# Kernel tuning notes

Hardware: AMD Instinct MI355X
Metric: run time of the kernel (lower is better)

Reference implementation:

```python
import jax, jax.numpy as jnp
import numpy as np

N = 50000
E = 800000
IN = 128
HID = 32
HEADS = 4
OUT = 32
NEG_SLOPE = 0.2  # PyG GATConv default


def setup_inputs() -> dict:
    key = jax.random.key(0)
    ks = jax.random.split(key, 16)
    s = lambda k, sh: jax.random.normal(k, sh, jnp.float32) * 0.05
    inp = {}
    inp["x"] = jax.random.normal(ks[0], (N, IN), jnp.float32)
    inp["edge_idx"] = jax.random.randint(ks[1], (2, E), 0, N)
    inp["edge_attr"] = jax.random.normal(ks[2], (E, 1), jnp.float32)
    inp["lin1_w"] = s(ks[3], (IN, HEADS * HID))
    inp["att1_src"] = s(ks[4], (HEADS, HID))
    inp["att1_dst"] = s(ks[5], (HEADS, HID))
    inp["lin1_edge_w"] = s(ks[6], (1, HEADS * HID))
    inp["att1_edge"] = s(ks[7], (HEADS, HID))
    inp["bias1"] = jnp.zeros((HEADS * HID,), jnp.float32)
    inp["lin2_w"] = s(ks[8], (HEADS * HID, OUT))
    inp["att2_src"] = s(ks[9], (1, OUT))
    inp["att2_dst"] = s(ks[10], (1, OUT))
    inp["lin2_edge_w"] = s(ks[11], (1, OUT))
    inp["att2_edge"] = s(ks[12], (1, OUT))
    inp["bias2"] = jnp.zeros((OUT,), jnp.float32)
    return inp


def _gat_conv(x, src, dst, eattr, lin_w, a_src, a_dst, lin_e, a_e, bias, heads, ch, concat):
    """PyG GATConv (eval mode): gather -> leaky_relu logits -> segment softmax over dst -> scatter-sum."""
    n = x.shape[0]
    xl = (x @ lin_w).reshape(n, heads, ch)                      # [N,H,C]
    alpha = ((xl * a_src).sum(-1)[src]                          # [Etot,H]
             + (xl * a_dst).sum(-1)[dst]
             + ((eattr @ lin_e).reshape(-1, heads, ch) * a_e).sum(-1))
    alpha = jax.nn.leaky_relu(alpha, NEG_SLOPE)
    amax = jax.ops.segment_max(alpha, dst, num_segments=n)      # every node has a self-loop
    ex = jnp.exp(alpha - amax[dst])
    den = jax.ops.segment_sum(ex, dst, num_segments=n)
    w = ex / den[dst]                                           # [Etot,H]
    out = jax.ops.segment_sum(w[:, :, None] * xl[src], dst, num_segments=n)  # [N,H,C]
    out = out.reshape(n, heads * ch) if concat else out.mean(axis=1)
    return out + bias


def reference(x, edge_idx, edge_attr,
              lin1_w, att1_src, att1_dst, lin1_edge_w, att1_edge, bias1,
              lin2_w, att2_src, att2_dst, lin2_edge_w, att2_edge, bias2):
    n = x.shape[0]
    # add_self_loops=True with edge_attr fill_value='mean' (PyG default when edge_dim is set)
    loops = jnp.arange(n)
    src = jnp.concatenate([edge_idx[0], loops])
    dst = jnp.concatenate([edge_idx[1], loops])
    ea = jnp.concatenate(
        [edge_attr, jnp.broadcast_to(edge_attr.mean(0, keepdims=True), (n, edge_attr.shape[1]))], 0)
    h = jax.nn.elu(_gat_conv(x, src, dst, ea, lin1_w, att1_src, att1_dst,
                             lin1_edge_w, att1_edge, bias1, HEADS, HID, True))
    # F.dropout with training=False -> identity (eval mode)
    return _gat_conv(h, src, dst, ea, lin2_w, att2_src, att2_dst,
                     lin2_edge_w, att2_edge, bias2, 1, OUT, True)
```

## Files before the change

### kernel.cpp

```cpp
#include <hip/hip_runtime.h>
#include <hip/hip_fp16.h>
#include <math.h>

#define NN   50000
#define EE   800000
#define ETOT 850000
#define NEG  0.2f
#define SCAN_BLOCKS ((NN + 255) / 256)

#define O_DEG    0
#define O_EASUM  50000
#define ZERO_ELEMS 50004
#define O_COEF   50004
#define O_ROWPTR 50012
#define O_CURSOR 100016
#define O_BLKSUM 150016
#define O_BLKOFF 150272
#define O_CSRSE  150528
#define O_ASRC1  1850528
#define O_ADST1  2050528
#define O_XLH    2250528
#define O_OUT1   5450528
#define O_HLH    11850528
#define O_ASRC2  12650528
#define O_ADST2  12700528
#define WS_ELEMS 12750528

__global__ __launch_bounds__(256) void k_ea_count(
    const float* __restrict__ ea, const int* __restrict__ ei,
    float* __restrict__ easum, int* __restrict__ deg) {
  __shared__ float red[4];
  int e = blockIdx.x * 256 + threadIdx.x;
  float s = 0.f;
  if (e < EE) {
    s = ea[e];
    atomicAdd(deg + ei[EE + e], 1);
  }
  #pragma unroll
  for (int o = 32; o > 0; o >>= 1) s += __shfl_down(s, o, 64);
  if ((threadIdx.x & 63) == 0) red[threadIdx.x >> 6] = s;
  __syncthreads();
  if (threadIdx.x == 0) atomicAdd(easum, red[0] + red[1] + red[2] + red[3]);
}

__global__ void k_coef(const float* __restrict__ lew1, const float* __restrict__ ae1,
                       const float* __restrict__ lew2, const float* __restrict__ ae2,
                       float* __restrict__ coef) {
  int t = threadIdx.x;
  float p = lew1[t] * ae1[t];
  #pragma unroll
  for (int o = 16; o > 0; o >>= 1) p += __shfl_down(p, o, 32);
  if ((t & 31) == 0) coef[t >> 5] = p;
  if (t < 32) {
    float q = lew2[t] * ae2[t];
    #pragma unroll
    for (int o = 16; o > 0; o >>= 1) q += __shfl_down(q, o, 32);
    if (t == 0) coef[4] = q;
  }
}

__device__ __forceinline__ int wave_incl_scan(int v, int lane) {
  #pragma unroll
  for (int o = 1; o < 64; o <<= 1) {
    int u = __shfl_up(v, o, 64);
    if (lane >= o) v += u;
  }
  return v;
}

__global__ __launch_bounds__(256) void k_scan_blk(const int* __restrict__ deg,
                                                  int* __restrict__ rowptr,
                                                  int* __restrict__ blksum) {
  __shared__ int wsum[4];
  const int t = threadIdx.x;
  const int i = blockIdx.x * 256 + t;
  const int lane = t & 63, wv = t >> 6;
  int v = (i < NN) ? (deg[i] + 1) : 0;
  int incl = wave_incl_scan(v, lane);
  if (lane == 63) wsum[wv] = incl;
  __syncthreads();
  int off = 0;
  #pragma unroll
  for (int k = 0; k < 4; ++k) if (k < wv) off += wsum[k];
  incl += off;
  if (i < NN) rowptr[i] = incl - v;
  if (t == 255) blksum[blockIdx.x] = incl;
}

__global__ __launch_bounds__(256) void k_scan_top(const int* __restrict__ blksum,
                                                  int* __restrict__ blkoff) {
  __shared__ int wsum[4];
  const int t = threadIdx.x;
  const int lane = t & 63, wv = t >> 6;
  int v = (t < SCAN_BLOCKS) ? blksum[t] : 0;
  int incl = wave_incl_scan(v, lane);
  if (lane == 63) wsum[wv] = incl;
  __syncthreads();
  int off = 0;
  #pragma unroll
  for (int k = 0; k < 4; ++k) if (k < wv) off += wsum[k];
  incl += off;
  if (t < SCAN_BLOCKS) blkoff[t] = incl - v;
}

__global__ __launch_bounds__(256) void k_scan_add(int* __restrict__ rowptr,
                                                  int* __restrict__ cursor,
                                                  const int* __restrict__ blkoff) {
  const int i = blockIdx.x * 256 + threadIdx.x;
  if (i < NN) {
    int r = rowptr[i] + blkoff[blockIdx.x];
    rowptr[i] = r;
    cursor[i] = r;
  }
  if (i == 0) rowptr[NN] = ETOT;
}

__global__ void k_fill(const int* __restrict__ ei, const float* __restrict__ eattr,
                       const float* __restrict__ easum, int* __restrict__ cursor,
                       uint2* __restrict__ csr_se) {
  int e = blockIdx.x * 256 + threadIdx.x;
  if (e >= ETOT) return;
  int s, d; float ea;
  if (e < EE) { s = ei[e]; d = ei[EE + e]; ea = eattr[e]; }
  else { s = d = e - EE; ea = easum[0] * (1.f / EE); }
  int slot = atomicAdd(cursor + d, 1);
  csr_se[slot] = make_uint2((unsigned)s, __float_as_uint(ea));
}

#define GEMM_STEP(WB, K, XS) {                                              \
    const float4* Wr = (const float4*)((WB) + (size_t)(K));                 \
    _Pragma("unroll")                                                       \
    for (int j4 = 0; j4 < 8; ++j4) {                                        \
      float4 wv = Wr[j4];                                                   \
      acc[j4 * 4 + 0] += (XS) * wv.x;                                       \
      acc[j4 * 4 + 1] += (XS) * wv.y;                                       \
      acc[j4 * 4 + 2] += (XS) * wv.z;                                       \
      acc[j4 * 4 + 3] += (XS) * wv.w;                                       \
    } }

#define L1_NB ((NN + 63) / 64)
__global__ __launch_bounds__(64) void k_lin1(
    const float* __restrict__ x, const float* __restrict__ W,
    const float* __restrict__ att_src, const float* __restrict__ att_dst,
    __half* __restrict__ xlh, float* __restrict__ asrc, float* __restrict__ adst) {
  const int bid = blockIdx.x;
  const int h   = bid / L1_NB;
  const int n   = (bid % L1_NB) * 64 + threadIdx.x;
  const int nc  = n < NN ? n : NN - 1;
  const float4* xr = (const float4*)(x + (size_t)nc * 128);
  const float*  Wh = W + h * 32;
  float acc[32];
  #pragma unroll
  for (int j = 0; j < 32; ++j) acc[j] = 0.f;
  float4 xv = xr[0];
  for (int kt = 0; kt < 32; ++kt) {
    float4 cur = xv;
    if (kt < 31) xv = xr[kt + 1];
    GEMM_STEP(Wh, (kt * 4 + 0) * 128, cur.x);
    GEMM_STEP(Wh, (kt * 4 + 1) * 128, cur.y);
    GEMM_STEP(Wh, (kt * 4 + 2) * 128, cur.z);
    GEMM_STEP(Wh, (kt * 4 + 3) * 128, cur.w);
  }
  if (n < NN) {
    __align__(16) __half hbuf[32];
    #pragma unroll
    for (int j = 0; j < 32; ++j) hbuf[j] = __float2half_rn(acc[j]);
    float4* dst = (float4*)(xlh + (size_t)n * 128 + h * 32);
    #pragma unroll
    for (int i = 0; i < 4; ++i) dst[i] = ((const float4*)hbuf)[i];
    float ss = 0.f, sd = 0.f;
    #pragma unroll
    for (int j = 0; j < 32; ++j) {
      ss += acc[j] * att_src[h * 32 + j];
      sd += acc[j] * att_dst[h * 32 + j];
    }
    asrc[n * 4 + h] = ss;
    adst[n * 4 + h] = sd;
  }
}

__global__ __launch_bounds__(256) void k_agg1(
    const int* __restrict__ rowptr, const uint2* __restrict__ csr_se,
    const float* __restrict__ asrc, const float* __restrict__ adst,
    const float* __restrict__ coef,
    const __half* __restrict__ xlh, float* __restrict__ out1) {
  int n = blockIdx.x * 8 + (threadIdx.x >> 5);
  if (n >= NN) return;
  int l = threadIdx.x & 31;
  int c4 = l << 2;
  int h = l >> 3;
  float cf = coef[h];
  float ad = adst[(size_t)n * 4 + h];
  int r0 = rowptr[n], r1 = rowptr[n + 1];
  float a0 = 0.f, a1 = 0.f, a2 = 0.f, a3 = 0.f, den = 0.f;
  for (int j = r0; j < r1; j += 4) {
    int sv[4]; float eav[4], asv[4]; uint2 raw[4];
    #pragma unroll
    for (int k = 0; k < 4; ++k) {
      int jj = (j + k < r1) ? (j + k) : (r1 - 1);
      uint2 se = csr_se[jj];
      sv[k] = (int)se.x;
      eav[k] = __uint_as_float(se.y);
    }
    #pragma unroll
    for (int k = 0; k < 4; ++k) {
      asv[k] = asrc[(size_t)sv[k] * 4 + h];
      raw[k] = *(const uint2*)(xlh + (size_t)sv[k] * 128 + c4);
    }
    #pragma unroll
    for (int k = 0; k < 4; ++k) {
      float alpha = asv[k] + ad + eav[k] * cf;
      alpha = alpha > 0.f ? alpha : NEG * alpha;
      float ex = (j + k < r1) ? __expf(alpha) : 0.f;
      __half2 p0, p1;
      *(unsigned int*)&p0 = raw[k].x;
      *(unsigned int*)&p1 = raw[k].y;
      float2 f0 = __half22float2(p0), f1 = __half22float2(p1);
      a0 += ex * f0.x;
      a1 += ex * f0.y;
      a2 += ex * f1.x;
      a3 += ex * f1.y;
      den += ex;
    }
  }
  float inv = 1.f / den;
  *(float4*)(out1 + (size_t)n * 128 + c4) = make_float4(a0 * inv, a1 * inv, a2 * inv, a3 * inv);
}

__global__ __launch_bounds__(64) void k_lin2(
    const float* __restrict__ out1, const float* __restrict__ bias1,
    const float* __restrict__ W2,
    const float* __restrict__ as2w, const float* __restrict__ ad2w,
    __half* __restrict__ hlh, float* __restrict__ asrc2, float* __restrict__ adst2) {
  const int n  = blockIdx.x * 64 + threadIdx.x;
  const int nc = n < NN ? n : NN - 1;
  const float4* xr = (const float4*)(out1 + (size_t)nc * 128);
  const float4* br = (const float4*)bias1;
  float acc[32];
  #pragma unroll
  for (int j = 0; j < 32; ++j) acc[j] = 0.f;
  float4 xv = xr[0];
  for (int kt = 0; kt < 32; ++kt) {
    float4 cur = xv;
    if (kt < 31) xv = xr[kt + 1];
    float4 b = br[kt];
    cur.x += b.x; cur.y += b.y; cur.z += b.z; cur.w += b.w;
    cur.x = cur.x > 0.f ? cur.x : (expf(cur.x) - 1.f);
    cur.y = cur.y > 0.f ? cur.y : (expf(cur.y) - 1.f);
    cur.z = cur.z > 0.f ? cur.z : (expf(cur.z) - 1.f);
    cur.w = cur.w > 0.f ? cur.w : (expf(cur.w) - 1.f);
    GEMM_STEP(W2, (kt * 4 + 0) * 32, cur.x);
    GEMM_STEP(W2, (kt * 4 + 1) * 32, cur.y);
    GEMM_STEP(W2, (kt * 4 + 2) * 32, cur.z);
    GEMM_STEP(W2, (kt * 4 + 3) * 32, cur.w);
  }
  if (n < NN) {
    __align__(16) __half hbuf[32];
    #pragma unroll
    for (int j = 0; j < 32; ++j) hbuf[j] = __float2half_rn(acc[j]);
    float4* dst = (float4*)(hlh + (size_t)n * 32);
    #pragma unroll
    for (int i = 0; i < 4; ++i) dst[i] = ((const float4*)hbuf)[i];
    float ps = 0.f, pd = 0.f;
    #pragma unroll
    for (int j = 0; j < 32; ++j) {
      ps += acc[j] * as2w[j];
      pd += acc[j] * ad2w[j];
    }
    asrc2[n] = ps;
    adst2[n] = pd;
  }
}

__global__ __launch_bounds__(256) void k_agg2(
    const int* __restrict__ rowptr, const uint2* __restrict__ csr_se,
    const float* __restrict__ asrc2, const float* __restrict__ adst2,
    const float* __restrict__ coef,
    const __half* __restrict__ hlh, const float* __restrict__ bias2,
    float* __restrict__ out) {
  int n = blockIdx.x * 32 + (threadIdx.x >> 3);
  if (n >= NN) return;
  int c4 = (threadIdx.x & 7) << 2;
  float cf = coef[4];
  float ad = adst2[n];
  int r0 = rowptr[n], r1 = rowptr[n + 1];
  float a0 = 0.f, a1 = 0.f, a2 = 0.f, a3 = 0.f, den = 0.f;
  for (int j = r0; j < r1; j += 4) {
    int sv[4]; float eav[4], asv[4]; uint2 raw[4];
    #pragma unroll
    for (int k = 0; k < 4; ++k) {
      int jj = (j + k < r1) ? (j + k) : (r1 - 1);
      uint2 se = csr_se[jj];
      sv[k] = (int)se.x;
      eav[k] = __uint_as_float(se.y);
    }
    #pragma unroll
    for (int k = 0; k < 4; ++k) {
      asv[k] = asrc2[sv[k]];
      raw[k] = *(const uint2*)(hlh + (size_t)sv[k] * 32 + c4);
    }
    #pragma unroll
    for (int k = 0; k < 4; ++k) {
      float alpha = asv[k] + ad + eav[k] * cf;
      alpha = alpha > 0.f ? alpha : NEG * alpha;
      float ex = (j + k < r1) ? __expf(alpha) : 0.f;
      __half2 p0, p1;
      *(unsigned int*)&p0 = raw[k].x;
      *(unsigned int*)&p1 = raw[k].y;
      float2 f0 = __half22float2(p0), f1 = __half22float2(p1);
      a0 += ex * f0.x;
      a1 += ex * f0.y;
      a2 += ex * f1.x;
      a3 += ex * f1.y;
      den += ex;
    }
  }
  float inv = 1.f / den;
  float4 b = *(const float4*)(bias2 + c4);
  *(float4*)(out + (size_t)n * 32 + c4) =
      make_float4(a0 * inv + b.x, a1 * inv + b.y, a2 * inv + b.z, a3 * inv + b.w);
}

extern "C" void kernel_launch(void* const* d_in, const int* in_sizes, int n_in,
                              void* d_out, int out_size, void* d_ws, size_t ws_size,
                              hipStream_t stream) {
  const float* x        = (const float*)d_in[0];
  const int*   ei       = (const int*)d_in[1];
  const float* eattr    = (const float*)d_in[2];
  const float* lin1_w   = (const float*)d_in[3];
  const float* att1_src = (const float*)d_in[4];
  const float* att1_dst = (const float*)d_in[5];
  const float* lin1_ew  = (const float*)d_in[6];
  const float* att1_e   = (const float*)d_in[7];
  const float* bias1    = (const float*)d_in[8];
  const float* lin2_w   = (const float*)d_in[9];
  const float* att2_src = (const float*)d_in[10];
  const float* att2_dst = (const float*)d_in[11];
  const float* lin2_ew  = (const float*)d_in[12];
  const float* att2_e   = (const float*)d_in[13];
  const float* bias2    = (const float*)d_in[14];
  float* out = (float*)d_out;
  float* ws  = (float*)d_ws;
  int*   wsi = (int*)d_ws;

  int*    deg     = wsi + O_DEG;
  float*  easum   = ws + O_EASUM;
  float*  coef    = ws + O_COEF;
  int*    rowptr  = wsi + O_ROWPTR;
  int*    cursor  = wsi + O_CURSOR;
  int*    blksum  = wsi + O_BLKSUM;
  int*    blkoff  = wsi + O_BLKOFF;
  uint2*  csr_se  = (uint2*)(wsi + O_CSRSE);
  float*  asrc1   = ws + O_ASRC1;
  float*  adst1   = ws + O_ADST1;
  __half* xlh     = (__half*)(ws + O_XLH);
  float*  out1    = ws + O_OUT1;
  __half* hlh     = (__half*)(ws + O_HLH);
  float*  asrc2   = ws + O_ASRC2;
  float*  adst2   = ws + O_ADST2;

  hipMemsetAsync(ws, 0, (size_t)ZERO_ELEMS * sizeof(float), stream);

  k_ea_count<<<(EE + 255) / 256, 256, 0, stream>>>(eattr, ei, easum, deg);
  k_coef<<<1, 128, 0, stream>>>(lin1_ew, att1_e, lin2_ew, att2_e, coef);

  k_scan_blk<<<SCAN_BLOCKS, 256, 0, stream>>>(deg, rowptr, blksum);
  k_scan_top<<<1, 256, 0, stream>>>(blksum, blkoff);
  k_scan_add<<<SCAN_BLOCKS, 256, 0, stream>>>(rowptr, cursor, blkoff);
  k_fill<<<(ETOT + 255) / 256, 256, 0, stream>>>(ei, eattr, easum, cursor, csr_se);

  k_lin1<<<L1_NB * 4, 64, 0, stream>>>(x, lin1_w, att1_src, att1_dst, xlh, asrc1, adst1);
  k_agg1<<<(NN + 7) / 8, 256, 0, stream>>>(rowptr, csr_se, asrc1, adst1, coef, xlh, out1);

  k_lin2<<<(NN + 63) / 64, 64, 0, stream>>>(out1, bias1, lin2_w, att2_src, att2_dst, hlh, asrc2, adst2);
  k_agg2<<<(NN + 31) / 32, 256, 0, stream>>>(rowptr, csr_se, asrc2, adst2, coef, hlh, bias2, out);
}
```

Baseline: 346.6 us.

## Fuse all GAT stages into one cooperative persistent kernel with grid syncs

Replaces the chain of separate launches (memset, degree count, coef, three-stage scan, CSR fill, lin1, agg1, lin2, agg2) with a single cooperative kernel whose phases are separated by grid-wide syncs. The degree-count atomics now also record each edge's rank, so CSR slots are computed directly and the fill needs no second atomic pass. That fill is interleaved per wave with the lin1 GEMM tasks so the two overlap. The CSR is split into separate source and edge-attribute arrays. The aim is to remove per-launch overhead and the extra atomic traffic. The cost is about nine grid barriers, occupancy capped by launch bounds, and two gathers per edge instead of one packed load.

```diff
diff --git a/kernel.cpp b/kernel.cpp
--- a/kernel.cpp
+++ b/kernel.cpp
@@ -1,63 +1,48 @@
 #include <hip/hip_runtime.h>
+#include <hip/hip_cooperative_groups.h>
 #include <hip/hip_fp16.h>
 #include <math.h>
+
+namespace cg = cooperative_groups;
 
 #define NN   50000
 #define EE   800000
 #define ETOT 850000
 #define NEG  0.2f
-#define SCAN_BLOCKS ((NN + 255) / 256)
+#define L1_NB 782
+#define L1_TASKS (L1_NB * 4)
+#define W_TASKS (L1_TASKS * 5)
 
 #define O_DEG    0
-#define O_EASUM  50000
-#define ZERO_ELEMS 50004
-#define O_COEF   50004
-#define O_ROWPTR 50012
-#define O_CURSOR 100016
-#define O_BLKSUM 150016
-#define O_BLKOFF 150272
-#define O_CSRSE  150528
-#define O_ASRC1  1850528
-#define O_ADST1  2050528
-#define O_XLH    2250528
-#define O_OUT1   5450528
-#define O_HLH    11850528
-#define O_ASRC2  12650528
-#define O_ADST2  12700528
-#define WS_ELEMS 12750528
-
-__global__ __launch_bounds__(256) void k_ea_count(
-    const float* __restrict__ ea, const int* __restrict__ ei,
-    float* __restrict__ easum, int* __restrict__ deg) {
-  __shared__ float red[4];
-  int e = blockIdx.x * 256 + threadIdx.x;
-  float s = 0.f;
-  if (e < EE) {
-    s = ea[e];
-    atomicAdd(deg + ei[EE + e], 1);
-  }
-  #pragma unroll
-  for (int o = 32; o > 0; o >>= 1) s += __shfl_down(s, o, 64);
-  if ((threadIdx.x & 63) == 0) red[threadIdx.x >> 6] = s;
-  __syncthreads();
-  if (threadIdx.x == 0) atomicAdd(easum, red[0] + red[1] + red[2] + red[3]);
-}
-
-__global__ void k_coef(const float* __restrict__ lew1, const float* __restrict__ ae1,
-                       const float* __restrict__ lew2, const float* __restrict__ ae2,
-                       float* __restrict__ coef) {
-  int t = threadIdx.x;
-  float p = lew1[t] * ae1[t];
-  #pragma unroll
-  for (int o = 16; o > 0; o >>= 1) p += __shfl_down(p, o, 32);
-  if ((t & 31) == 0) coef[t >> 5] = p;
-  if (t < 32) {
-    float q = lew2[t] * ae2[t];
-    #pragma unroll
-    for (int o = 16; o > 0; o >>= 1) q += __shfl_down(q, o, 32);
-    if (t == 0) coef[4] = q;
-  }
-}
+#define O_EAPART 50000
+#define O_BLKSUM 52048
+#define O_BLKOFF 54096
+#define O_COEF   56144
+#define O_ROWPTR 56152
+#define O_RANK   106156
+#define O_CSRSRC 906156
+#define O_EASLOT 1756156
+#define O_ASRC1  2606156
+#define O_ADST1  2806156
+#define O_XLH    3006156
+#define O_OUT1   6206156
+#define O_HLH    12606156
+#define O_ASRC2  13406156
+#define O_ADST2  13456156
+#define WS_ELEMS 13506156
+
+struct MegaParams {
+  const float* x; const int* ei; const float* eattr;
+  const float* W1; const float* a1s; const float* a1d;
+  const float* lew1; const float* ae1; const float* bias1;
+  const float* W2; const float* a2s; const float* a2d;
+  const float* lew2; const float* ae2; const float* bias2;
+  float* out;
+  int* deg; float* eapart; int* blksum; int* blkoff; float* coef;
+  int* rowptr; int* rank; int* csr_src; float* ea_slot;
+  float* asrc1; float* adst1; __half* xlh; float* out1;
+  __half* hlh; float* asrc2; float* adst2;
+};
 
 __device__ __forceinline__ int wave_incl_scan(int v, int lane) {
   #pragma unroll
@@ -68,310 +53,344 @@
   return v;
 }
 
-__global__ __launch_bounds__(256) void k_scan_blk(const int* __restrict__ deg,
-                                                  int* __restrict__ rowptr,
-                                                  int* __restrict__ blksum) {
-  __shared__ int wsum[4];
-  const int t = threadIdx.x;
-  const int i = blockIdx.x * 256 + t;
-  const int lane = t & 63, wv = t >> 6;
-  int v = (i < NN) ? (deg[i] + 1) : 0;
-  int incl = wave_incl_scan(v, lane);
-  if (lane == 63) wsum[wv] = incl;
-  __syncthreads();
-  int off = 0;
-  #pragma unroll
-  for (int k = 0; k < 4; ++k) if (k < wv) off += wsum[k];
-  incl += off;
-  if (i < NN) rowptr[i] = incl - v;
-  if (t == 255) blksum[blockIdx.x] = incl;
-}
-
-__global__ __launch_bounds__(256) void k_scan_top(const int* __restrict__ blksum,
-                                                  int* __restrict__ blkoff) {
-  __shared__ int wsum[4];
-  const int t = threadIdx.x;
-  const int lane = t & 63, wv = t >> 6;
-  int v = (t < SCAN_BLOCKS) ? blksum[t] : 0;
-  int incl = wave_incl_scan(v, lane);
-  if (lane == 63) wsum[wv] = incl;
-  __syncthreads();
-  int off = 0;
-  #pragma unroll
-  for (int k = 0; k < 4; ++k) if (k < wv) off += wsum[k];
-  incl += off;
-  if (t < SCAN_BLOCKS) blkoff[t] = incl - v;
-}
-
-__global__ __launch_bounds__(256) void k_scan_add(int* __restrict__ rowptr,
-                                                  int* __restrict__ cursor,
-                                                  const int* __restrict__ blkoff) {
-  const int i = blockIdx.x * 256 + threadIdx.x;
-  if (i < NN) {
-    int r = rowptr[i] + blkoff[blockIdx.x];
-    rowptr[i] = r;
-    cursor[i] = r;
-  }
-  if (i == 0) rowptr[NN] = ETOT;
-}
-
-__global__ void k_fill(const int* __restrict__ ei, const float* __restrict__ eattr,
-                       const float* __restrict__ easum, int* __restrict__ cursor,
-                       uint2* __restrict__ csr_se) {
-  int e = blockIdx.x * 256 + threadIdx.x;
-  if (e >= ETOT) return;
-  int s, d; float ea;
-  if (e < EE) { s = ei[e]; d = ei[EE + e]; ea = eattr[e]; }
-  else { s = d = e - EE; ea = easum[0] * (1.f / EE); }
-  int slot = atomicAdd(cursor + d, 1);
-  csr_se[slot] = make_uint2((unsigned)s, __float_as_uint(ea));
-}
-
 #define GEMM_STEP(WB, K, XS) {                                              \
     const float4* Wr = (const float4*)((WB) + (size_t)(K));                 \
     _Pragma("unroll")                                                       \
     for (int j4 = 0; j4 < 8; ++j4) {                                        \
-      float4 wv = Wr[j4];                                                   \
-      acc[j4 * 4 + 0] += (XS) * wv.x;                                       \
-      acc[j4 * 4 + 1] += (XS) * wv.y;                                       \
-      acc[j4 * 4 + 2] += (XS) * wv.z;                                       \
-      acc[j4 * 4 + 3] += (XS) * wv.w;                                       \
+      float4 wv2 = Wr[j4];                                                  \
+      acc[j4 * 4 + 0] += (XS) * wv2.x;                                      \
+      acc[j4 * 4 + 1] += (XS) * wv2.y;                                      \
+      acc[j4 * 4 + 2] += (XS) * wv2.z;                                      \
+      acc[j4 * 4 + 3] += (XS) * wv2.w;                                      \
     } }
 
-#define L1_NB ((NN + 63) / 64)
-__global__ __launch_bounds__(64) void k_lin1(
-    const float* __restrict__ x, const float* __restrict__ W,
-    const float* __restrict__ att_src, const float* __restrict__ att_dst,
-    __half* __restrict__ xlh, float* __restrict__ asrc, float* __restrict__ adst) {
+__global__ __launch_bounds__(256, 4) void k_mega(MegaParams p) {
+  cg::grid_group gg = cg::this_grid();
+  __shared__ int   wsum[4];
+  __shared__ float fred[4];
+  const int t = threadIdx.x;
   const int bid = blockIdx.x;
-  const int h   = bid / L1_NB;
-  const int n   = (bid % L1_NB) * 64 + threadIdx.x;
-  const int nc  = n < NN ? n : NN - 1;
-  const float4* xr = (const float4*)(x + (size_t)nc * 128);
-  const float*  Wh = W + h * 32;
-  float acc[32];
-  #pragma unroll
-  for (int j = 0; j < 32; ++j) acc[j] = 0.f;
-  float4 xv = xr[0];
-  for (int kt = 0; kt < 32; ++kt) {
-    float4 cur = xv;
-    if (kt < 31) xv = xr[kt + 1];
-    GEMM_STEP(Wh, (kt * 4 + 0) * 128, cur.x);
-    GEMM_STEP(Wh, (kt * 4 + 1) * 128, cur.y);
-    GEMM_STEP(Wh, (kt * 4 + 2) * 128, cur.z);
-    GEMM_STEP(Wh, (kt * 4 + 3) * 128, cur.w);
-  }
-  if (n < NN) {
-    __align__(16) __half hbuf[32];
+  const int nblk = (int)gridDim.x;
+  const int gsz = nblk * 256;
+  const int gid = bid * 256 + t;
+  const int lane = t & 63, wv = t >> 6;
+
+  for (int i = gid; i < NN; i += gsz) p.deg[i] = 0;
+  gg.sync();
+
+  {
+    float s = 0.f;
+    for (int e = gid; e < EE; e += gsz) {
+      s += p.eattr[e];
+      p.rank[e] = atomicAdd(p.deg + p.ei[EE + e], 1);
+    }
     #pragma unroll
-    for (int j = 0; j < 32; ++j) hbuf[j] = __float2half_rn(acc[j]);
-    float4* dst = (float4*)(xlh + (size_t)n * 128 + h * 32);
+    for (int o = 32; o > 0; o >>= 1) s += __shfl_down(s, o, 64);
+    if (lane == 0) fred[wv] = s;
+    __syncthreads();
+    if (t == 0) p.eapart[bid] = fred[0] + fred[1] + fred[2] + fred[3];
+  }
+  gg.sync();
+
+  if (bid == 0) {
+    float fs = 0.f;
+    for (int i = t; i < nblk; i += 256) fs += p.eapart[i];
     #pragma unroll
-    for (int i = 0; i < 4; ++i) dst[i] = ((const float4*)hbuf)[i];
-    float ss = 0.f, sd = 0.f;
+    for (int o = 32; o > 0; o >>= 1) fs += __shfl_down(fs, o, 64);
+    __syncthreads();
+    if (lane == 0) fred[wv] = fs;
+    __syncthreads();
+    if (t == 0) p.coef[5] = (fred[0] + fred[1] + fred[2] + fred[3]) * (1.f / EE);
+    if (t < 128) {
+      float pp = p.lew1[t] * p.ae1[t];
+      #pragma unroll
+      for (int o = 16; o > 0; o >>= 1) pp += __shfl_down(pp, o, 32);
+      if ((t & 31) == 0) p.coef[t >> 5] = pp;
+      if (t < 32) {
+        float q = p.lew2[t] * p.ae2[t];
+        #pragma unroll
+        for (int o = 16; o > 0; o >>= 1) q += __shfl_down(q, o, 32);
+        if (t == 0) p.coef[4] = q;
+      }
+    }
+  }
+  gg.sync();
+
+  {
+    int i = gid;
+    int v = (i < NN) ? p.deg[i] + 1 : 0;
+    int incl = wave_incl_scan(v, lane);
+    if (lane == 63) wsum[wv] = incl;
+    __syncthreads();
+    int off = 0;
     #pragma unroll
-    for (int j = 0; j < 32; ++j) {
-      ss += acc[j] * att_src[h * 32 + j];
-      sd += acc[j] * att_dst[h * 32 + j];
-    }
-    asrc[n * 4 + h] = ss;
-    adst[n * 4 + h] = sd;
-  }
-}
-
-__global__ __launch_bounds__(256) void k_agg1(
-    const int* __restrict__ rowptr, const uint2* __restrict__ csr_se,
-    const float* __restrict__ asrc, const float* __restrict__ adst,
-    const float* __restrict__ coef,
-    const __half* __restrict__ xlh, float* __restrict__ out1) {
-  int n = blockIdx.x * 8 + (threadIdx.x >> 5);
-  if (n >= NN) return;
-  int l = threadIdx.x & 31;
-  int c4 = l << 2;
-  int h = l >> 3;
-  float cf = coef[h];
-  float ad = adst[(size_t)n * 4 + h];
-  int r0 = rowptr[n], r1 = rowptr[n + 1];
-  float a0 = 0.f, a1 = 0.f, a2 = 0.f, a3 = 0.f, den = 0.f;
-  for (int j = r0; j < r1; j += 4) {
-    int sv[4]; float eav[4], asv[4]; uint2 raw[4];
-    #pragma unroll
-    for (int k = 0; k < 4; ++k) {
-      int jj = (j + k < r1) ? (j + k) : (r1 - 1);
-      uint2 se = csr_se[jj];
-      sv[k] = (int)se.x;
-      eav[k] = __uint_as_float(se.y);
-    }
-    #pragma unroll
-    for (int k = 0; k < 4; ++k) {
-      asv[k] = asrc[(size_t)sv[k] * 4 + h];
-      raw[k] = *(const uint2*)(xlh + (size_t)sv[k] * 128 + c4);
-    }
-    #pragma unroll
-    for (int k = 0; k < 4; ++k) {
-      float alpha = asv[k] + ad + eav[k] * cf;
-      alpha = alpha > 0.f ? alpha : NEG * alpha;
-      float ex = (j + k < r1) ? __expf(alpha) : 0.f;
-      __half2 p0, p1;
-      *(unsigned int*)&p0 = raw[k].x;
-      *(unsigned int*)&p1 = raw[k].y;
-      float2 f0 = __half22float2(p0), f1 = __half22float2(p1);
-      a0 += ex * f0.x;
-      a1 += ex * f0.y;
-      a2 += ex * f1.x;
-      a3 += ex * f1.y;
-      den += ex;
-    }
-  }
-  float inv = 1.f / den;
-  *(float4*)(out1 + (size_t)n * 128 + c4) = make_float4(a0 * inv, a1 * inv, a2 * inv, a3 * inv);
-}
-
-__global__ __launch_bounds__(64) void k_lin2(
-    const float* __restrict__ out1, const float* __restrict__ bias1,
-    const float* __restrict__ W2,
-    const float* __restrict__ as2w, const float* __restrict__ ad2w,
-    __half* __restrict__ hlh, float* __restrict__ asrc2, float* __restrict__ adst2) {
-  const int n  = blockIdx.x * 64 + threadIdx.x;
-  const int nc = n < NN ? n : NN - 1;
-  const float4* xr = (const float4*)(out1 + (size_t)nc * 128);
-  const float4* br = (const float4*)bias1;
-  float acc[32];
-  #pragma unroll
-  for (int j = 0; j < 32; ++j) acc[j] = 0.f;
-  float4 xv = xr[0];
-  for (int kt = 0; kt < 32; ++kt) {
-    float4 cur = xv;
-    if (kt < 31) xv = xr[kt + 1];
-    float4 b = br[kt];
-    cur.x += b.x; cur.y += b.y; cur.z += b.z; cur.w += b.w;
-    cur.x = cur.x > 0.f ? cur.x : (expf(cur.x) - 1.f);
-    cur.y = cur.y > 0.f ? cur.y : (expf(cur.y) - 1.f);
-    cur.z = cur.z > 0.f ? cur.z : (expf(cur.z) - 1.f);
-    cur.w = cur.w > 0.f ? cur.w : (expf(cur.w) - 1.f);
-    GEMM_STEP(W2, (kt * 4 + 0) * 32, cur.x);
-    GEMM_STEP(W2, (kt * 4 + 1) * 32, cur.y);
-    GEMM_STEP(W2, (kt * 4 + 2) * 32, cur.z);
-    GEMM_STEP(W2, (kt * 4 + 3) * 32, cur.w);
-  }
-  if (n < NN) {
-    __align__(16) __half hbuf[32];
-    #pragma unroll
-    for (int j = 0; j < 32; ++j) hbuf[j] = __float2half_rn(acc[j]);
-    float4* dst = (float4*)(hlh + (size_t)n * 32);
-    #pragma unroll
-    for (int i = 0; i < 4; ++i) dst[i] = ((const float4*)hbuf)[i];
-    float ps = 0.f, pd = 0.f;
-    #pragma unroll
-    for (int j = 0; j < 32; ++j) {
-      ps += acc[j] * as2w[j];
-      pd += acc[j] * ad2w[j];
-    }
-    asrc2[n] = ps;
-    adst2[n] = pd;
-  }
-}
-
-__global__ __launch_bounds__(256) void k_agg2(
-    const int* __restrict__ rowptr, const uint2* __restrict__ csr_se,
-    const float* __restrict__ asrc2, const float* __restrict__ adst2,
-    const float* __restrict__ coef,
-    const __half* __restrict__ hlh, const float* __restrict__ bias2,
-    float* __restrict__ out) {
-  int n = blockIdx.x * 32 + (threadIdx.x >> 3);
-  if (n >= NN) return;
-  int c4 = (threadIdx.x & 7) << 2;
-  float cf = coef[4];
-  float ad = adst2[n];
-  int r0 = rowptr[n], r1 = rowptr[n + 1];
-  float a0 = 0.f, a1 = 0.f, a2 = 0.f, a3 = 0.f, den = 0.f;
-  for (int j = r0; j < r1; j += 4) {
-    int sv[4]; float eav[4], asv[4]; uint2 raw[4];
-    #pragma unroll
-    for (int k = 0; k < 4; ++k) {
-      int jj = (j + k < r1) ? (j + k) : (r1 - 1);
-      uint2 se = csr_se[jj];
-      sv[k] = (int)se.x;
-      eav[k] = __uint_as_float(se.y);
-    }
-    #pragma unroll
-    for (int k = 0; k < 4; ++k) {
-      asv[k] = asrc2[sv[k]];
-      raw[k] = *(const uint2*)(hlh + (size_t)sv[k] * 32 + c4);
-    }
-    #pragma unroll
-    for (int k = 0; k < 4; ++k) {
-      float alpha = asv[k] + ad + eav[k] * cf;
-      alpha = alpha > 0.f ? alpha : NEG * alpha;
-      float ex = (j + k < r1) ? __expf(alpha) : 0.f;
-      __half2 p0, p1;
-      *(unsigned int*)&p0 = raw[k].x;
-      *(unsigned int*)&p1 = raw[k].y;
-      float2 f0 = __half22float2(p0), f1 = __half22float2(p1);
-      a0 += ex * f0.x;
-      a1 += ex * f0.y;
-      a2 += ex * f1.x;
-      a3 += ex * f1.y;
-      den += ex;
-    }
-  }
-  float inv = 1.f / den;
-  float4 b = *(const float4*)(bias2 + c4);
-  *(float4*)(out + (size_t)n * 32 + c4) =
-      make_float4(a0 * inv + b.x, a1 * inv + b.y, a2 * inv + b.z, a3 * inv + b.w);
+    for (int k = 0; k < 4; ++k) if (k < wv) off += wsum[k];
+    incl += off;
+    if (i < NN) p.rowptr[i] = incl - v;
+    if (t == 255) p.blksum[bid] = incl;
+  }
+  gg.sync();
+
+  if (bid == 0) {
+    int carry = 0;
+    for (int c0 = 0; c0 < nblk; c0 += 256) {
+      __syncthreads();
+      int i = c0 + t;
+      int v = (i < nblk) ? p.blksum[i] : 0;
+      int incl = wave_incl_scan(v, lane);
+      if (lane == 63) wsum[wv] = incl;
+      __syncthreads();
+      int off = 0, tot = 0;
+      #pragma unroll
+      for (int k = 0; k < 4; ++k) { int w = wsum[k]; tot += w; if (k < wv) off += w; }
+      if (i < nblk) p.blkoff[i] = carry + incl + off - v;
+      carry += tot;
+    }
+  }
+  gg.sync();
+
+  {
+    int i = gid;
+    if (i < NN) {
+      int r = p.rowptr[i] + p.blkoff[bid];
+      p.rowptr[i] = r;
+      int slot = r + p.deg[i];
+      p.csr_src[slot] = i;
+      p.ea_slot[slot] = p.coef[5];
+    }
+    if (gid == 0) p.rowptr[NN] = ETOT;
+  }
+  gg.sync();
+
+  for (int wt = bid * 4 + wv; wt < W_TASKS; wt += nblk * 4) {
+    int g5 = wt / 5, r5 = wt % 5;
+    if (r5 != 0) {
+      int e = (g5 * 4 + r5 - 1) * 64 + lane;
+      if (e < EE) {
+        int s = p.ei[e];
+        int d = p.ei[EE + e];
+        float ea = p.eattr[e];
+        int slot = p.rowptr[d] + p.rank[e];
+        p.csr_src[slot] = s;
+        p.ea_slot[slot] = ea;
+      }
+    } else {
+      int h = g5 / L1_NB;
+      int n = (g5 % L1_NB) * 64 + lane;
+      int nc = n < NN ? n : NN - 1;
+      const float4* xr = (const float4*)(p.x + (size_t)nc * 128);
+      const float* Wh = p.W1 + h * 32;
+      float acc[32];
+      #pragma unroll
+      for (int j = 0; j < 32; ++j) acc[j] = 0.f;
+      float4 xv = xr[0];
+      for (int kt = 0; kt < 32; ++kt) {
+        float4 cur = xv;
+        if (kt < 31) xv = xr[kt + 1];
+        GEMM_STEP(Wh, (kt * 4 + 0) * 128, cur.x);
+        GEMM_STEP(Wh, (kt * 4 + 1) * 128, cur.y);
+        GEMM_STEP(Wh, (kt * 4 + 2) * 128, cur.z);
+        GEMM_STEP(Wh, (kt * 4 + 3) * 128, cur.w);
+      }
+      if (n < NN) {
+        __align__(16) __half hbuf[32];
+        #pragma unroll
+        for (int j = 0; j < 32; ++j) hbuf[j] = __float2half_rn(acc[j]);
+        float4* dst = (float4*)(p.xlh + (size_t)n * 128 + h * 32);
+        #pragma unroll
+        for (int i4 = 0; i4 < 4; ++i4) dst[i4] = ((const float4*)hbuf)[i4];
+        float ss = 0.f, sd = 0.f;
+        #pragma unroll
+        for (int j = 0; j < 32; ++j) {
+          ss += acc[j] * p.a1s[h * 32 + j];
+          sd += acc[j] * p.a1d[h * 32 + j];
+        }
+        p.asrc1[n * 4 + h] = ss;
+        p.adst1[n * 4 + h] = sd;
+      }
+    }
+  }
+  gg.sync();
+
+  for (int nb2 = bid; nb2 < NN / 8; nb2 += nblk) {
+    int n = nb2 * 8 + (t >> 5);
+    int l = t & 31;
+    int c4 = l << 2;
+    int h = l >> 3;
+    float cf = p.coef[h];
+    float ad = p.adst1[(size_t)n * 4 + h];
+    int r0 = p.rowptr[n], r1 = p.rowptr[n + 1];
+    float a0 = 0.f, a1 = 0.f, a2 = 0.f, a3 = 0.f, den = 0.f;
+    for (int j = r0; j < r1; j += 4) {
+      int sv[4]; float eav[4], asv[4]; uint2 raw[4];
+      #pragma unroll
+      for (int k = 0; k < 4; ++k) {
+        int jj = (j + k < r1) ? (j + k) : (r1 - 1);
+        sv[k] = p.csr_src[jj];
+        eav[k] = p.ea_slot[jj];
+      }
+      #pragma unroll
+      for (int k = 0; k < 4; ++k) {
+        asv[k] = p.asrc1[(size_t)sv[k] * 4 + h];
+        raw[k] = *(const uint2*)(p.xlh + (size_t)sv[k] * 128 + c4);
+      }
+      #pragma unroll
+      for (int k = 0; k < 4; ++k) {
+        float alpha = asv[k] + ad + eav[k] * cf;
+        alpha = alpha > 0.f ? alpha : NEG * alpha;
+        float ex = (j + k < r1) ? __expf(alpha) : 0.f;
+        __half2 p0, p1;
+        *(unsigned int*)&p0 = raw[k].x;
+        *(unsigned int*)&p1 = raw[k].y;
+        float2 f0 = __half22float2(p0), f1 = __half22float2(p1);
+        a0 += ex * f0.x;
+        a1 += ex * f0.y;
+        a2 += ex * f1.x;
+        a3 += ex * f1.y;
+        den += ex;
+      }
+    }
+    float inv = 1.f / den;
+    *(float4*)(p.out1 + (size_t)n * 128 + c4) =
+        make_float4(a0 * inv, a1 * inv, a2 * inv, a3 * inv);
+  }
+  gg.sync();
+
+  {
+    int n = gid;
+    int nc = n < NN ? n : NN - 1;
+    if (gid < ((NN + 63) / 64) * 64) {
+      const float4* xr = (const float4*)(p.out1 + (size_t)nc * 128);
+      const float4* br = (const float4*)p.bias1;
+      float acc[32];
+      #pragma unroll
+      for (int j = 0; j < 32; ++j) acc[j] = 0.f;
+      float4 xv = xr[0];
+      for (int kt = 0; kt < 32; ++kt) {
+        float4 cur = xv;
+        if (kt < 31) xv = xr[kt + 1];
+        float4 b = br[kt];
+        cur.x += b.x; cur.y += b.y; cur.z += b.z; cur.w += b.w;
+        cur.x = cur.x > 0.f ? cur.x : (__expf(cur.x) - 1.f);
+        cur.y = cur.y > 0.f ? cur.y : (__expf(cur.y) - 1.f);
+        cur.z = cur.z > 0.f ? cur.z : (__expf(cur.z) - 1.f);
+        cur.w = cur.w > 0.f ? cur.w : (__expf(cur.w) - 1.f);
+        GEMM_STEP(p.W2, (kt * 4 + 0) * 32, cur.x);
+        GEMM_STEP(p.W2, (kt * 4 + 1) * 32, cur.y);
+        GEMM_STEP(p.W2, (kt * 4 + 2) * 32, cur.z);
+        GEMM_STEP(p.W2, (kt * 4 + 3) * 32, cur.w);
+      }
+      if (n < NN) {
+        __align__(16) __half hbuf[32];
+        #pragma unroll
+        for (int j = 0; j < 32; ++j) hbuf[j] = __float2half_rn(acc[j]);
+        float4* dst = (float4*)(p.hlh + (size_t)n * 32);
+        #pragma unroll
+        for (int i4 = 0; i4 < 4; ++i4) dst[i4] = ((const float4*)hbuf)[i4];
+        float ps = 0.f, pd = 0.f;
+        #pragma unroll
+        for (int j = 0; j < 32; ++j) {
+          ps += acc[j] * p.a2s[j];
+          pd += acc[j] * p.a2d[j];
+        }
+        p.asrc2[n] = ps;
+        p.adst2[n] = pd;
+      }
+    }
+  }
+  gg.sync();
+
+  for (int nb2 = bid; nb2 < (NN + 31) / 32; nb2 += nblk) {
+    int n = nb2 * 32 + (t >> 3);
+    if (n < NN) {
+      int c4 = (t & 7) << 2;
+      float cf = p.coef[4];
+      float ad = p.adst2[n];
+      int r0 = p.rowptr[n], r1 = p.rowptr[n + 1];
+      float a0 = 0.f, a1 = 0.f, a2 = 0.f, a3 = 0.f, den = 0.f;
+      for (int j = r0; j < r1; j += 4) {
+        int sv[4]; float eav[4], asv[4]; uint2 raw[4];
+        #pragma unroll
+        for (int k = 0; k < 4; ++k) {
+          int jj = (j + k < r1) ? (j + k) : (r1 - 1);
+          sv[k] = p.csr_src[jj];
+          eav[k] = p.ea_slot[jj];
+        }
+        #pragma unroll
+        for (int k = 0; k < 4; ++k) {
+          asv[k] = p.asrc2[sv[k]];
+          raw[k] = *(const uint2*)(p.hlh + (size_t)sv[k] * 32 + c4);
+        }
+        #pragma unroll
+        for (int k = 0; k < 4; ++k) {
+          float alpha = asv[k] + ad + eav[k] * cf;
+          alpha = alpha > 0.f ? alpha : NEG * alpha;
+          float ex = (j + k < r1) ? __expf(alpha) : 0.f;
+          __half2 p0, p1;
+          *(unsigned int*)&p0 = raw[k].x;
+          *(unsigned int*)&p1 = raw[k].y;
+          float2 f0 = __half22float2(p0), f1 = __half22float2(p1);
+          a0 += ex * f0.x;
+          a1 += ex * f0.y;
+          a2 += ex * f1.x;
+          a3 += ex * f1.y;
+          den += ex;
+        }
+      }
+      float inv = 1.f / den;
+      float4 b = *(const float4*)(p.bias2 + c4);
+      *(float4*)(p.out + (size_t)n * 32 + c4) =
+          make_float4(a0 * inv + b.x, a1 * inv + b.y, a2 * inv + b.z, a3 * inv + b.w);
+    }
+  }
 }
 
 extern "C" void kernel_launch(void* const* d_in, const int* in_sizes, int n_in,
                               void* d_out, int out_size, void* d_ws, size_t ws_size,
                               hipStream_t stream) {
-  const float* x        = (const float*)d_in[0];
-  const int*   ei       = (const int*)d_in[1];
-  const float* eattr    = (const float*)d_in[2];
-  const float* lin1_w   = (const float*)d_in[3];
-  const float* att1_src = (const float*)d_in[4];
-  const float* att1_dst = (const float*)d_in[5];
-  const float* lin1_ew  = (const float*)d_in[6];
-  const float* att1_e   = (const float*)d_in[7];
-  const float* bias1    = (const float*)d_in[8];
-  const float* lin2_w   = (const float*)d_in[9];
-  const float* att2_src = (const float*)d_in[10];
-  const float* att2_dst = (const float*)d_in[11];
-  const float* lin2_ew  = (const float*)d_in[12];
-  const float* att2_e   = (const float*)d_in[13];
-  const float* bias2    = (const float*)d_in[14];
-  float* out = (float*)d_out;
-  float* ws  = (float*)d_ws;
+  float* ws = (float*)d_ws;
   int*   wsi = (int*)d_ws;
 
-  int*    deg     = wsi + O_DEG;
-  float*  easum   = ws + O_EASUM;
-  float*  coef    = ws + O_COEF;
-  int*    rowptr  = wsi + O_ROWPTR;
-  int*    cursor  = wsi + O_CURSOR;
-  int*    blksum  = wsi + O_BLKSUM;
-  int*    blkoff  = wsi + O_BLKOFF;
-  uint2*  csr_se  = (uint2*)(wsi + O_CSRSE);
-  float*  asrc1   = ws + O_ASRC1;
-  float*  adst1   = ws + O_ADST1;
-  __half* xlh     = (__half*)(ws + O_XLH);
-  float*  out1    = ws + O_OUT1;
-  __half* hlh     = (__half*)(ws + O_HLH);
-  float*  asrc2   = ws + O_ASRC2;
-  float*  adst2   = ws + O_ADST2;
-
-  hipMemsetAsync(ws, 0, (size_t)ZERO_ELEMS * sizeof(float), stream);
-
-  k_ea_count<<<(EE + 255) / 256, 256, 0, stream>>>(eattr, ei, easum, deg);
-  k_coef<<<1, 128, 0, stream>>>(lin1_ew, att1_e, lin2_ew, att2_e, coef);
-
-  k_scan_blk<<<SCAN_BLOCKS, 256, 0, stream>>>(deg, rowptr, blksum);
-  k_scan_top<<<1, 256, 0, stream>>>(blksum, blkoff);
-  k_scan_add<<<SCAN_BLOCKS, 256, 0, stream>>>(rowptr, cursor, blkoff);
-  k_fill<<<(ETOT + 255) / 256, 256, 0, stream>>>(ei, eattr, easum, cursor, csr_se);
-
-  k_lin1<<<L1_NB * 4, 64, 0, stream>>>(x, lin1_w, att1_src, att1_dst, xlh, asrc1, adst1);
-  k_agg1<<<(NN + 7) / 8, 256, 0, stream>>>(rowptr, csr_se, asrc1, adst1, coef, xlh, out1);
-
-  k_lin2<<<(NN + 63) / 64, 64, 0, stream>>>(out1, bias1, lin2_w, att2_src, att2_dst, hlh, asrc2, adst2);
-  k_agg2<<<(NN + 31) / 32, 256, 0, stream>>>(rowptr, csr_se, asrc2, adst2, coef, hlh, bias2, out);
+  MegaParams p;
+  p.x     = (const float*)d_in[0];
+  p.ei    = (const int*)d_in[1];
+  p.eattr = (const float*)d_in[2];
+  p.W1    = (const float*)d_in[3];
+  p.a1s   = (const float*)d_in[4];
+  p.a1d   = (const float*)d_in[5];
+  p.lew1  = (const float*)d_in[6];
+  p.ae1   = (const float*)d_in[7];
+  p.bias1 = (const float*)d_in[8];
+  p.W2    = (const float*)d_in[9];
+  p.a2s   = (const float*)d_in[10];
+  p.a2d   = (const float*)d_in[11];
+  p.lew2  = (const float*)d_in[12];
+  p.ae2   = (const float*)d_in[13];
+  p.bias2 = (const float*)d_in[14];
+  p.out   = (float*)d_out;
+  p.deg     = wsi + O_DEG;
+  p.eapart  = ws + O_EAPART;
+  p.blksum  = wsi + O_BLKSUM;
+  p.blkoff  = wsi + O_BLKOFF;
+  p.coef    = ws + O_COEF;
+  p.rowptr  = wsi + O_ROWPTR;
+  p.rank    = wsi + O_RANK;
+  p.csr_src = wsi + O_CSRSRC;
+  p.ea_slot = ws + O_EASLOT;
+  p.asrc1   = ws + O_ASRC1;
+  p.adst1   = ws + O_ADST1;
+  p.xlh     = (__half*)(ws + O_XLH);
+  p.out1    = ws + O_OUT1;
+  p.hlh     = (__half*)(ws + O_HLH);
+  p.asrc2   = ws + O_ASRC2;
+  p.adst2   = ws + O_ADST2;
+
+  int bpc = 0;
+  hipError_t err = hipOccupancyMaxActiveBlocksPerMultiprocessor(&bpc, (const void*)k_mega, 256, 0);
+  if (err != hipSuccess || bpc <= 0) bpc = 2;
+  if (bpc > 8) bpc = 8;
+  dim3 grid(bpc * 256);
+  dim3 block(256);
+  void* args[] = { &p };
+  hipLaunchCooperativeKernel((const void*)k_mega, grid, block, args, 0, stream);
 }
```

New measurement: 929.4 us. 168% more time.
